# Kernel tuning notes

Hardware: AMD Instinct MI355X
Metric: run time of the kernel (lower is better)

## Reference

```python
import jax, jax.numpy as jnp
from jax import lax
import numpy as np

N_POINTS = 2_000_000
EXTENT = 512          # fine voxel extent per axis
STRIDE = 16           # pool kernel/stride
G = EXTENT // STRIDE  # coarse grid per axis = 32
C_IN = 3
C_OUT = 64
K = 3                 # conv kernel size


def setup_inputs() -> dict:
    key = jax.random.key(0)
    k1, k2, k3 = jax.random.split(key, 3)
    coords = jax.random.randint(k1, (N_POINTS, 3), 0, EXTENT, dtype=jnp.int32)
    feats = jax.random.normal(k2, (N_POINTS, C_IN), dtype=jnp.float32)
    # MinkowskiConvolution kernel (no bias by default): [out, in, kD, kH, kW]
    fan_in = C_IN * K ** 3
    W = jax.random.normal(k3, (C_OUT, C_IN, K, K, K), dtype=jnp.float32) / np.sqrt(fan_in)
    return {"coords": coords, "feats": feats, "W": W}


def reference(coords, feats, W):
    # --- MinkowskiAvgPooling(kernel=16, stride=16) ---
    # coarse voxel id per point; average of features of occupied fine voxels in block
    cid = coords // STRIDE                               # [N,3] in [0,G)
    idx = (cid[:, 0] * G + cid[:, 1]) * G + cid[:, 2]    # [N] linearized coarse id
    n_seg = G * G * G
    sums = jax.ops.segment_sum(feats, idx, num_segments=n_seg)               # [G^3,Cin]
    cnt = jax.ops.segment_sum(jnp.ones((feats.shape[0], 1), feats.dtype), idx,
                              num_segments=n_seg)                            # [G^3,1]
    avg = sums / jnp.maximum(cnt, 1.0)                   # zeros at empty coarse voxels

    # --- MinkowskiConvolution(Cin->Cout, k=3, stride=1) on coarse sparse grid ---
    # Empty neighbors contribute zero features, so a dense SAME conv over the
    # zero-filled coarse grid matches the sparse kernel-map gather.
    grid = avg.reshape(1, G, G, G, C_IN).transpose(0, 4, 1, 2, 3)   # NCDHW
    conv = lax.conv_general_dilated(
        grid, W, window_strides=(1, 1, 1), padding="SAME",
        dimension_numbers=("NCDHW", "OIDHW", "NCDHW"))               # [1,Cout,G,G,G]
    # conv outputs only at occupied coarse coords (Minkowski semantics)
    occ = (cnt > 0).astype(conv.dtype).reshape(1, 1, G, G, G)
    conv = conv * occ

    # --- MinkowskiPoolingTranspose(kernel=16, stride=16) ---
    # broadcast each coarse feature back to the occupied fine coords in its block
    flat = conv.transpose(0, 2, 3, 4, 1).reshape(n_seg, C_OUT)       # [G^3,Cout]
    out = flat[idx]                                                  # [N,Cout]
    return out
```

## Files before the change

### kernel.cpp

```cpp
#include <hip/hip_runtime.h>

#define G 32
#define NCELL (G * G * G)
#define C_IN 3
#define C_OUT 64
#define PBLK 64
#define HTHREADS 1024

typedef float     f32x4  __attribute__((ext_vector_type(4)));
typedef int       i32x4  __attribute__((ext_vector_type(4)));
typedef _Float16  f16x4v __attribute__((ext_vector_type(4)));
typedef _Float16  f16x8v __attribute__((ext_vector_type(8)));


__global__ void cellid_kernel(const i32x4* __restrict__ coords4,
                              int* __restrict__ cellid, int n) {
    int t = blockIdx.x * blockDim.x + threadIdx.x;
    int base = t * 4;
    if (base >= n) return;
    i32x4 a = coords4[t * 3 + 0];
    i32x4 b = coords4[t * 3 + 1];
    i32x4 c = coords4[t * 3 + 2];
    int c0 = (((a.x >> 4) * G + (a.y >> 4)) * G + (a.z >> 4));
    int c1 = (((a.w >> 4) * G + (b.x >> 4)) * G + (b.y >> 4));
    int c2 = (((b.z >> 4) * G + (b.w >> 4)) * G + (c.x >> 4));
    int c3 = (((c.y >> 4) * G + (c.z >> 4)) * G + (c.w >> 4));
    if (base + 3 < n) {
        i32x4 r = {c0, c1, c2, c3};
        *(i32x4*)&cellid[base] = r;
    } else {
        cellid[base] = c0;
        if (base + 1 < n) cellid[base + 1] = c1;
        if (base + 2 < n) cellid[base + 2] = c2;
    }
}

__global__ __launch_bounds__(HTHREADS) void histo_kernel(
    const int* __restrict__ cellid,
    const float* __restrict__ feats,
    float* __restrict__ partial,
    int n, int ppc) {
    __shared__ __align__(16) float h[NCELL];
    int vtype = blockIdx.x & 3;
    int chunk = blockIdx.x >> 2;

    f32x4* h4 = (f32x4*)h;
    for (int t = threadIdx.x; t < NCELL / 4; t += HTHREADS)
        h4[t] = (f32x4){0.f, 0.f, 0.f, 0.f};
    __syncthreads();

    int start = chunk * ppc;
    int end = start + ppc; if (end > n) end = n;
    if (vtype < 3) {
        for (int i = start + threadIdx.x; i < end; i += HTHREADS) {
            int c = cellid[i];
            atomicAdd(&h[c], feats[i * 3 + vtype]);
        }
    } else {
        for (int i = start + threadIdx.x; i < end; i += HTHREADS) {
            int c = cellid[i];
            atomicAdd(&h[c], 1.0f);
        }
    }
    __syncthreads();

    f32x4* pp = (f32x4*)(partial + ((size_t)vtype * PBLK + chunk) * NCELL);
    for (int t = threadIdx.x; t < NCELL / 4; t += HTHREADS)
        pp[t] = h4[t];
}

__global__ void reduce_kernel(const float* __restrict__ partial,
                              float* __restrict__ avg) {
    int cell = blockIdx.x * blockDim.x + threadIdx.x;
    if (cell >= NCELL) return;
    float s0 = 0.f, s1 = 0.f, s2 = 0.f, c = 0.f;
    for (int p = 0; p < PBLK; ++p) {
        s0 += partial[((size_t)0 * PBLK + p) * NCELL + cell];
        s1 += partial[((size_t)1 * PBLK + p) * NCELL + cell];
        s2 += partial[((size_t)2 * PBLK + p) * NCELL + cell];
        c  += partial[((size_t)3 * PBLK + p) * NCELL + cell];
    }
    float inv = c > 0.f ? 1.0f / c : 0.f;
    avg[cell * 3 + 0] = s0 * inv;
    avg[cell * 3 + 1] = s1 * inv;
    avg[cell * 3 + 2] = s2 * inv;
}

__global__ void conv_half_kernel(const float* __restrict__ avg,
                                 const float* __restrict__ W,
                                 _Float16* __restrict__ tab) {
    __shared__ float wlds[C_OUT * C_IN * 27];
    for (int t = threadIdx.x; t < C_OUT * C_IN * 27; t += blockDim.x)
        wlds[t] = W[t];
    __syncthreads();

    int cell = blockIdx.x * blockDim.x + threadIdx.x;
    if (cell >= NCELL) return;
    int z = cell & 31;
    int y = (cell >> 5) & 31;
    int x = cell >> 10;

    float acc[C_OUT];
#pragma unroll
    for (int c = 0; c < C_OUT; ++c) acc[c] = 0.f;

    for (int kd = 0; kd < 3; ++kd) {
        int nx = x + kd - 1;
        if (nx < 0 || nx >= G) continue;
        for (int kh = 0; kh < 3; ++kh) {
            int ny = y + kh - 1;
            if (ny < 0 || ny >= G) continue;
            for (int kw = 0; kw < 3; ++kw) {
                int nz = z + kw - 1;
                if (nz < 0 || nz >= G) continue;
                int nc = (nx * G + ny) * G + nz;
                float g0 = avg[nc * 3 + 0];
                float g1 = avg[nc * 3 + 1];
                float g2 = avg[nc * 3 + 2];
                int koff = (kd * 3 + kh) * 3 + kw;
#pragma unroll
                for (int co = 0; co < C_OUT; ++co) {
                    const float* wp = &wlds[co * C_IN * 27 + koff];
                    acc[co] += wp[0] * g0 + wp[27] * g1 + wp[54] * g2;
                }
            }
        }
    }
    f16x8v* dst = (f16x8v*)&tab[(size_t)cell * C_OUT];
#pragma unroll
    for (int q = 0; q < 8; ++q) {
        f16x8v p;
#pragma unroll
        for (int e = 0; e < 8; ++e) p[e] = (_Float16)acc[q * 8 + e];
        dst[q] = p;
    }
}

__global__ void gather_half_kernel(const int* __restrict__ cellid,
                                   const f16x4v* __restrict__ tab,
                                   f32x4* __restrict__ out, int n) {
    long g = (long)blockIdx.x * blockDim.x + threadIdx.x;
    int i = (int)(g >> 4);
    int c4 = (int)(g & 15);
    if (i >= n) return;
    int cell = cellid[i];
    f16x4v v = tab[(size_t)cell * 16 + c4];
    f32x4 o = {(float)v[0], (float)v[1], (float)v[2], (float)v[3]};
    __builtin_nontemporal_store(o, &out[(size_t)i * 16 + c4]);
}

__global__ void scatter_atomic_kernel(const int* __restrict__ coords,
                                      const float* __restrict__ feats,
                                      float* __restrict__ sums,
                                      float* __restrict__ cnt, int n) {
    int i = blockIdx.x * blockDim.x + threadIdx.x;
    if (i >= n) return;
    int x = coords[i * 3 + 0] >> 4;
    int y = coords[i * 3 + 1] >> 4;
    int z = coords[i * 3 + 2] >> 4;
    int cell = (x * G + y) * G + z;
    atomicAdd(&sums[cell * 3 + 0], feats[i * 3 + 0]);
    atomicAdd(&sums[cell * 3 + 1], feats[i * 3 + 1]);
    atomicAdd(&sums[cell * 3 + 2], feats[i * 3 + 2]);
    atomicAdd(&cnt[cell], 1.0f);
}

__global__ void avg_kernel(const float* __restrict__ sums,
                           const float* __restrict__ cnt,
                           float* __restrict__ avg) {
    int cell = blockIdx.x * blockDim.x + threadIdx.x;
    if (cell >= NCELL) return;
    float c = cnt[cell];
    float inv = c > 0.f ? 1.0f / c : 0.f;
    avg[cell * 3 + 0] = sums[cell * 3 + 0] * inv;
    avg[cell * 3 + 1] = sums[cell * 3 + 1] * inv;
    avg[cell * 3 + 2] = sums[cell * 3 + 2] * inv;
}

__global__ void conv_kernel(const float* __restrict__ avg,
                            const float* __restrict__ W,
                            float* __restrict__ convout) {
    __shared__ float wlds[C_OUT * C_IN * 27];
    for (int t = threadIdx.x; t < C_OUT * C_IN * 27; t += blockDim.x)
        wlds[t] = W[t];
    __syncthreads();

    int cell = blockIdx.x * blockDim.x + threadIdx.x;
    if (cell >= NCELL) return;
    int z = cell & 31;
    int y = (cell >> 5) & 31;
    int x = cell >> 10;

    float acc[C_OUT];
#pragma unroll
    for (int c = 0; c < C_OUT; ++c) acc[c] = 0.f;

    for (int kd = 0; kd < 3; ++kd) {
        int nx = x + kd - 1;
        if (nx < 0 || nx >= G) continue;
        for (int kh = 0; kh < 3; ++kh) {
            int ny = y + kh - 1;
            if (ny < 0 || ny >= G) continue;
            for (int kw = 0; kw < 3; ++kw) {
                int nz = z + kw - 1;
                if (nz < 0 || nz >= G) continue;
                int nc = (nx * G + ny) * G + nz;
                float g0 = avg[nc * 3 + 0];
                float g1 = avg[nc * 3 + 1];
                float g2 = avg[nc * 3 + 2];
                int koff = (kd * 3 + kh) * 3 + kw;
#pragma unroll
                for (int co = 0; co < C_OUT; ++co) {
                    const float* wp = &wlds[co * C_IN * 27 + koff];
                    acc[co] += wp[0] * g0 + wp[27] * g1 + wp[54] * g2;
                }
            }
        }
    }
    float* op = &convout[(size_t)cell * C_OUT];
#pragma unroll
    for (int co = 0; co < C_OUT; ++co) op[co] = acc[co];
}

__global__ void gather_coords_kernel(const int* __restrict__ coords,
                                     const f32x4* __restrict__ convout,
                                     f32x4* __restrict__ out, int n) {
    long g = (long)blockIdx.x * blockDim.x + threadIdx.x;
    int i = (int)(g >> 4);
    int c4 = (int)(g & 15);
    if (i >= n) return;
    int x = coords[i * 3 + 0] >> 4;
    int y = coords[i * 3 + 1] >> 4;
    int z = coords[i * 3 + 2] >> 4;
    int cell = (x * G + y) * G + z;
    out[(size_t)i * 16 + c4] = convout[(size_t)cell * 16 + c4];
}

extern "C" void kernel_launch(void* const* d_in, const int* in_sizes, int n_in,
                              void* d_out, int out_size, void* d_ws, size_t ws_size,
                              hipStream_t stream) {
    const int*   coords = (const int*)d_in[0];
    const float* feats  = (const float*)d_in[1];
    const float* W      = (const float*)d_in[2];
    float* out = (float*)d_out;
    int n = in_sizes[0] / 3;

    float*    sums    = (float*)d_ws;
    float*    cnt     = sums + NCELL * 3;
    float*    avg     = cnt + NCELL;
    float*    convout = avg + NCELL * 3;
    _Float16* tabh    = (_Float16*)(convout + (size_t)NCELL * 64);
    int*      cellid  = (int*)((float*)tabh + (size_t)NCELL * 32);
    float*    partial = (float*)(cellid + ((n + 3) & ~3));

    size_t need = ((size_t)NCELL * (3 + 1 + 3 + 64 + 32) + ((n + 3) & ~3) +
                   (size_t)4 * PBLK * NCELL) * 4;
    bool fast = (ws_size >= need);

    long total = (long)n * 16;
    if (fast) {
        int npt4 = (n + 3) / 4;
        cellid_kernel<<<(npt4 + 255) / 256, 256, 0, stream>>>(
            (const i32x4*)coords, cellid, n);
        int ppc = (n + PBLK - 1) / PBLK;
        histo_kernel<<<4 * PBLK, HTHREADS, 0, stream>>>(cellid, feats, partial, n, ppc);
        reduce_kernel<<<NCELL / 256, 256, 0, stream>>>(partial, avg);
        conv_half_kernel<<<NCELL / 256, 256, 0, stream>>>(avg, W, tabh);
        gather_half_kernel<<<(int)((total + 255) / 256), 256, 0, stream>>>(
            cellid, (const f16x4v*)tabh, (f32x4*)out, n);
    } else {
        hipMemsetAsync(d_ws, 0, NCELL * 4 * sizeof(float), stream);
        scatter_atomic_kernel<<<(n + 255) / 256, 256, 0, stream>>>(coords, feats, sums, cnt, n);
        avg_kernel<<<NCELL / 256, 256, 0, stream>>>(sums, cnt, avg);
        conv_kernel<<<NCELL / 256, 256, 0, stream>>>(avg, W, convout);
        gather_coords_kernel<<<(int)((total + 255) / 256), 256, 0, stream>>>(
            coords, (const f32x4*)convout, (f32x4*)out, n);
    }
}
```

Baseline: 201.1 us.

## Batch gather over multiple points per thread and remap histogram block indices

The gather kernel now has each thread handle four points spaced npg apart. It issues their cellid loads (nontemporal) and table loads together before storing, to expose more memory-level parallelism. The histogram kernel remaps block indices so the four value types of a chunk are spread differently across the launch order, likely to balance blocks across XCDs. The reduce and conv kernels switch to 128-thread blocks to launch more blocks. The strided point assignment makes each warp's stores less contiguous across iterations and raises register use.

Result: slower. 260.5 us (+29.5%).

```diff
diff --git a/kernel.cpp b/kernel.cpp
--- a/kernel.cpp
+++ b/kernel.cpp
@@ -6,6 +6,7 @@
 #define C_OUT 64
 #define PBLK 64
 #define HTHREADS 1024
+#define GITER 4
 
 typedef float     f32x4  __attribute__((ext_vector_type(4)));
 typedef int       i32x4  __attribute__((ext_vector_type(4)));
@@ -41,8 +42,10 @@
     float* __restrict__ partial,
     int n, int ppc) {
     __shared__ __align__(16) float h[NCELL];
-    int vtype = blockIdx.x & 3;
-    int chunk = blockIdx.x >> 2;
+    int x = blockIdx.x & 7;
+    int s = blockIdx.x >> 3;
+    int chunk = x * 8 + (s >> 2);
+    int vtype = s & 3;
 
     f32x4* h4 = (f32x4*)h;
     for (int t = threadIdx.x; t < NCELL / 4; t += HTHREADS)
@@ -138,15 +141,34 @@
 
 __global__ void gather_half_kernel(const int* __restrict__ cellid,
                                    const f16x4v* __restrict__ tab,
-                                   f32x4* __restrict__ out, int n) {
+                                   f32x4* __restrict__ out, int n, int npg) {
     long g = (long)blockIdx.x * blockDim.x + threadIdx.x;
-    int i = (int)(g >> 4);
     int c4 = (int)(g & 15);
-    if (i >= n) return;
-    int cell = cellid[i];
-    f16x4v v = tab[(size_t)cell * 16 + c4];
-    f32x4 o = {(float)v[0], (float)v[1], (float)v[2], (float)v[3]};
-    __builtin_nontemporal_store(o, &out[(size_t)i * 16 + c4]);
+    int pb = (int)(g >> 4);
+    if (pb >= npg) return;
+
+    int  cells[GITER];
+    int  pidx[GITER];
+    bool val[GITER];
+#pragma unroll
+    for (int j = 0; j < GITER; ++j) {
+        int p = pb + j * npg;
+        pidx[j] = p;
+        val[j] = (p < n);
+        cells[j] = val[j] ? __builtin_nontemporal_load(&cellid[p]) : 0;
+    }
+    f16x4v v[GITER];
+#pragma unroll
+    for (int j = 0; j < GITER; ++j)
+        v[j] = tab[(size_t)cells[j] * 16 + c4];
+#pragma unroll
+    for (int j = 0; j < GITER; ++j) {
+        if (val[j]) {
+            f32x4 o = {(float)v[j][0], (float)v[j][1],
+                       (float)v[j][2], (float)v[j][3]};
+            __builtin_nontemporal_store(o, &out[(size_t)pidx[j] * 16 + c4]);
+        }
+    }
 }
 
 __global__ void scatter_atomic_kernel(const int* __restrict__ coords,
@@ -257,22 +279,24 @@
                    (size_t)4 * PBLK * NCELL) * 4;
     bool fast = (ws_size >= need);
 
-    long total = (long)n * 16;
     if (fast) {
         int npt4 = (n + 3) / 4;
         cellid_kernel<<<(npt4 + 255) / 256, 256, 0, stream>>>(
             (const i32x4*)coords, cellid, n);
         int ppc = (n + PBLK - 1) / PBLK;
         histo_kernel<<<4 * PBLK, HTHREADS, 0, stream>>>(cellid, feats, partial, n, ppc);
-        reduce_kernel<<<NCELL / 256, 256, 0, stream>>>(partial, avg);
-        conv_half_kernel<<<NCELL / 256, 256, 0, stream>>>(avg, W, tabh);
-        gather_half_kernel<<<(int)((total + 255) / 256), 256, 0, stream>>>(
-            cellid, (const f16x4v*)tabh, (f32x4*)out, n);
+        reduce_kernel<<<NCELL / 128, 128, 0, stream>>>(partial, avg);
+        conv_half_kernel<<<NCELL / 128, 128, 0, stream>>>(avg, W, tabh);
+        int npg = (n + GITER - 1) / GITER;
+        long gthreads = (long)npg * 16;
+        gather_half_kernel<<<(int)((gthreads + 255) / 256), 256, 0, stream>>>(
+            cellid, (const f16x4v*)tabh, (f32x4*)out, n, npg);
     } else {
         hipMemsetAsync(d_ws, 0, NCELL * 4 * sizeof(float), stream);
         scatter_atomic_kernel<<<(n + 255) / 256, 256, 0, stream>>>(coords, feats, sums, cnt, n);
         avg_kernel<<<NCELL / 256, 256, 0, stream>>>(sums, cnt, avg);
         conv_kernel<<<NCELL / 256, 256, 0, stream>>>(avg, W, convout);
+        long total = (long)n * 16;
         gather_coords_kernel<<<(int)((total + 255) / 256), 256, 0, stream>>>(
             coords, (const f32x4*)convout, (f32x4*)out, n);
     }
```
